# Kernel tuning notes

Measured on AMD Instinct MI355X. Metric: run time of the kernel, lower is better.

## Reference

```python
import jax, jax.numpy as jnp
import numpy as np

D_MODEL = 768
D_STATE = 16
D_CONV = 4
EXPAND = 2
D_INNER = D_MODEL * EXPAND
B, L = 2, 2048


def _silu(x):
    return x * jax.nn.sigmoid(x)


def _ssm_core(xn, inw, cw, cb, xw, dtw, dtb, Alog, Dp, outw):
    """Mamba selective SSM. xn: [B,L,d_model] -> [B,L,d_model]."""
    Bn, Ln, _ = xn.shape
    S = Alog.shape[1]
    d_inner = Alog.shape[0]
    k = cw.shape[-1]
    xz = xn @ inw                      # [B,L,2*d_inner]
    xi, z = jnp.split(xz, 2, axis=-1)
    # depthwise causal conv along L (torch pads both sides then slices [:L] == left-pad k-1)
    xc = jnp.swapaxes(xi, 1, 2)        # [B,d_inner,L]
    xc = jax.lax.conv_general_dilated(xc, cw, (1,), [(k - 1, 0)],
                                      feature_group_count=d_inner)
    xc = xc + cb[None, :, None]
    xc = _silu(jnp.swapaxes(xc, 1, 2))  # [B,L,d_inner]
    bcdt = xc @ xw                     # [B,L,1+2S]
    dt_raw = bcdt[..., :1]
    Bs = bcdt[..., 1:1 + S]            # [B,L,S]
    Cs = bcdt[..., 1 + S:]             # [B,L,S]
    dt = jax.nn.softplus(dt_raw * dtw[None, None, :] + dtb)  # [B,L,d_inner]
    A = -jnp.exp(jnp.clip(Alog, -6.0, 6.0))                  # [d_inner,S]
    dA = jnp.exp(dt[..., None] * A[None, None])               # [B,L,d_inner,S]
    dBx = dt[..., None] * Bs[:, :, None, :] * xc[..., None]   # [B,L,d_inner,S]

    def step(h, ins):
        dA_t, dBx_t, C_t = ins
        h = jnp.clip(dA_t * h + dBx_t, -10000.0, 10000.0)
        return h, jnp.einsum('bds,bs->bd', h, C_t)

    h0 = jnp.zeros((Bn, d_inner, S), xc.dtype)
    _, ys = jax.lax.scan(step, h0, (jnp.moveaxis(dA, 1, 0),
                                    jnp.moveaxis(dBx, 1, 0),
                                    jnp.moveaxis(Cs, 1, 0)))
    y = jnp.moveaxis(ys, 0, 1) + xc * Dp[None, None]
    y = y * _silu(z)
    return y @ outw


def setup_inputs() -> dict:
    key = jax.random.key(0)
    ks = jax.random.split(key, 20)
    def core_params(koff):
        return dict(
            inw=jax.random.normal(ks[koff + 0], (D_MODEL, 2 * D_INNER), jnp.float32) * 0.02,
            cw=jax.random.normal(ks[koff + 1], (D_INNER, 1, D_CONV), jnp.float32) * 0.2,
            cb=jnp.zeros((D_INNER,), jnp.float32),
            xw=jax.random.normal(ks[koff + 2], (D_INNER, 1 + 2 * D_STATE), jnp.float32) * 0.02,
            dtw=jax.random.normal(ks[koff + 3], (D_INNER,), jnp.float32) * 0.5,
            dtb=jax.random.normal(ks[koff + 4], (D_INNER,), jnp.float32) * 0.1,
            Alog=jnp.clip(jnp.log(jnp.arange(1, D_STATE + 1, dtype=jnp.float32))[None, :]
                          * jnp.ones((D_INNER, 1), jnp.float32), -6.0, 6.0),
            D=jnp.ones((D_INNER,), jnp.float32),
            outw=jax.random.normal(ks[koff + 5], (D_INNER, D_MODEL), jnp.float32) * 0.02,
        )
    f = core_params(2)
    b = core_params(8)
    return {
        'x': jax.random.normal(ks[0], (B, L, D_MODEL), jnp.float32),
        'ln_g': jnp.ones((D_MODEL,), jnp.float32),
        'ln_b': jnp.zeros((D_MODEL,), jnp.float32),
        'alpha': jnp.zeros((), jnp.float32),
        'f_inw': f['inw'], 'f_cw': f['cw'], 'f_cb': f['cb'], 'f_xw': f['xw'],
        'f_dtw': f['dtw'], 'f_dtb': f['dtb'], 'f_Alog': f['Alog'], 'f_D': f['D'], 'f_outw': f['outw'],
        'b_inw': b['inw'], 'b_cw': b['cw'], 'b_cb': b['cb'], 'b_xw': b['xw'],
        'b_dtw': b['dtw'], 'b_dtb': b['dtb'], 'b_Alog': b['Alog'], 'b_D': b['D'], 'b_outw': b['outw'],
    }


def reference(x, ln_g, ln_b, alpha,
              f_inw, f_cw, f_cb, f_xw, f_dtw, f_dtb, f_Alog, f_D, f_outw,
              b_inw, b_cw, b_cb, b_xw, b_dtw, b_dtb, b_Alog, b_D, b_outw):
    residual = x.astype(jnp.float32)
    mu = residual.mean(-1, keepdims=True)
    var = ((residual - mu) ** 2).mean(-1, keepdims=True)
    xn = (residual - mu) / jnp.sqrt(var + 1e-5) * ln_g + ln_b
    y_fwd = _ssm_core(xn, f_inw, f_cw, f_cb, f_xw, f_dtw, f_dtb, f_Alog, f_D, f_outw)
    y_bwd = jnp.flip(_ssm_core(jnp.flip(xn, 1), b_inw, b_cw, b_cb, b_xw,
                               b_dtw, b_dtb, b_Alog, b_D, b_outw), 1)
    a = jax.nn.sigmoid(alpha)
    y = a * y_fwd + (1.0 - a) * y_bwd
    return y + residual
```

## Files before the change

### kernel.cpp

```cpp
#include <hip/hip_runtime.h>
#include <cstddef>
#include <cstdint>

#define DMODEL 768
#define DINNER 1536
#define NSTATE 16
#define LSEQ   2048
#define NB     2
#define NTOK   (NB*LSEQ)
#define NBCDT  33

#define TC     32
#define NCHUNK (LSEQ/TC)
#define KSPLIT 12
#define LOG2E  1.44269504f

typedef __bf16 bf16x8 __attribute__((ext_vector_type(8)));
typedef float  floatx4 __attribute__((ext_vector_type(4)));

__device__ __forceinline__ float exp2_hw(float x) { return __builtin_amdgcn_exp2f(x); }
__device__ __forceinline__ float silu_f(float x) { return x / (1.f + expf(-x)); }
__device__ __forceinline__ float clip1e4(float x) {
    return __builtin_amdgcn_fmed3f(x, -1e4f, 1e4f);
}
__device__ __forceinline__ unsigned short f2bf(float f) {
    unsigned int u = __float_as_uint(f);
    unsigned int r = u + 0x7fffu + ((u >> 16) & 1u);
    return (unsigned short)(r >> 16);
}
__device__ __forceinline__ float bf2f(unsigned short u) {
    return __uint_as_float((unsigned int)u << 16);
}
__device__ __forceinline__ unsigned int pack2bf(float a, float b) {
    unsigned int ua = __float_as_uint(a); ua = ua + 0x7fffu + ((ua >> 16) & 1u);
    unsigned int ub = __float_as_uint(b); ub = ub + 0x7fffu + ((ub >> 16) & 1u);
    return (ua >> 16) | (ub & 0xffff0000u);
}
__device__ __forceinline__ void ld_lds16(unsigned short* lds, const unsigned short* g) {
    __builtin_amdgcn_global_load_lds(
        (const __attribute__((address_space(1))) unsigned int*)g,
        (__attribute__((address_space(3))) unsigned int*)lds,
        16, 0, 0);
}

__global__ void ln_kernel(const float* __restrict__ x,
                          const float* __restrict__ g,
                          const float* __restrict__ be,
                          unsigned short* __restrict__ xnb,
                          float* __restrict__ bcdt) {
    int row = blockIdx.x;
    int tid = threadIdx.x;
    int zi = row * 256 + tid;
    if (zi < 2 * NTOK * NBCDT) bcdt[zi] = 0.f;
    const float* xr = x + (size_t)row * DMODEL;
    float s = 0.f, ss = 0.f;
    for (int i = tid; i < DMODEL; i += 256) {
        float v = xr[i];
        s += v; ss += v * v;
    }
    for (int o = 32; o >= 1; o >>= 1) {
        s  += __shfl_xor(s,  o, 64);
        ss += __shfl_xor(ss, o, 64);
    }
    __shared__ float sS[4], sSS[4];
    int w = tid >> 6;
    if ((tid & 63) == 0) { sS[w] = s; sSS[w] = ss; }
    __syncthreads();
    s  = sS[0] + sS[1] + sS[2] + sS[3];
    ss = sSS[0] + sSS[1] + sSS[2] + sSS[3];
    float mu = s / DMODEL;
    float var = ss / DMODEL - mu * mu;
    float rstd = rsqrtf(var + 1e-5f);
    unsigned short* xo = xnb + (size_t)row * DMODEL;
    for (int i = tid; i < DMODEL; i += 256)
        xo[i] = f2bf((xr[i] - mu) * rstd * g[i] + be[i]);
}

__global__ __launch_bounds__(256)
void cast_weights(const float* __restrict__ f_inw, const float* __restrict__ b_inw,
                  const float* __restrict__ f_outw, const float* __restrict__ b_outw,
                  const float* __restrict__ f_xw, const float* __restrict__ b_xw,
                  const float* __restrict__ alpha,
                  unsigned short* __restrict__ inwT, unsigned short* __restrict__ outwT,
                  unsigned short* __restrict__ xwT) {
    __shared__ float t[32][33];
    int bid = blockIdx.x;
    int tid = threadIdx.x;
    int lr = tid >> 5, lc = tid & 31;
    if (bid < 4608) {
        int n0 = (bid % 192) * 32;
        int k0 = (bid / 192) * 32;
        const float* w = (n0 >= 3072) ? b_inw : f_inw;
        int nb = (n0 >= 3072) ? (n0 - 3072) : n0;
        #pragma unroll
        for (int r = 0; r < 4; r++)
            t[r * 8 + lr][lc] = w[(size_t)(k0 + r * 8 + lr) * 3072 + nb + lc];
        __syncthreads();
        #pragma unroll
        for (int r = 0; r < 4; r++)
            inwT[(size_t)(n0 + r * 8 + lr) * DMODEL + k0 + lc] = f2bf(t[lc][r * 8 + lr]);
    } else if (bid < 6912) {
        bid -= 4608;
        float a = 1.f / (1.f + expf(-alpha[0]));
        int n0 = (bid % 24) * 32;
        int k0 = (bid / 24) * 32;
        const float* w = (k0 >= DINNER) ? b_outw : f_outw;
        float sc = (k0 >= DINNER) ? (1.f - a) : a;
        int kb = (k0 >= DINNER) ? (k0 - DINNER) : k0;
        #pragma unroll
        for (int r = 0; r < 4; r++)
            t[r * 8 + lr][lc] = w[(size_t)(kb + r * 8 + lr) * DMODEL + n0 + lc];
        __syncthreads();
        #pragma unroll
        for (int r = 0; r < 4; r++)
            outwT[(size_t)(n0 + r * 8 + lr) * 3072 + k0 + lc] = f2bf(sc * t[lc][r * 8 + lr]);
    } else {
        bid -= 6912;
        int dir = bid / 48;
        int k0 = (bid % 48) * 32;
        const float* xw = dir ? b_xw : f_xw;
        unsigned short* dst = xwT + (size_t)dir * 48 * DINNER;
        for (int idx = tid; idx < 48 * 32; idx += 256) {
            int n = idx >> 5, kk = idx & 31;
            float v = (n < 33) ? xw[(size_t)(k0 + kk) * 33 + n] : 0.f;
            dst[(size_t)n * DINNER + k0 + kk] = f2bf(v);
        }
    }
}

__global__ __launch_bounds__(256)
void gemm_xz_mfma(const unsigned short* __restrict__ xnb,
                  const unsigned short* __restrict__ inwT,
                  unsigned short* __restrict__ xi, unsigned short* __restrict__ sz) {
    __shared__ unsigned short SH[2][2 * 128 * 64];
    int tid = threadIdx.x;
    int bm = blockIdx.y * 128;
    int bn = blockIdx.x * 128;
    int wave = tid >> 6, lane = tid & 63;
    int wm = (wave & 1) * 64, wn = (wave >> 1) * 64;
    int col15 = lane & 15, quad = lane >> 4;
    int lrow = lane >> 3;
    int lk   = (((lane & 7) ^ lrow) * 8);
    floatx4 acc[4][4];
    #pragma unroll
    for (int i = 0; i < 4; i++)
        #pragma unroll
        for (int j = 0; j < 4; j++)
            acc[i][j] = (floatx4){0.f, 0.f, 0.f, 0.f};

    int sw = col15 & 7;

#define STAGE_XZ(buf, k0)                                                       \
    {                                                                           \
        unsigned short* Abuf = SH[buf];                                         \
        unsigned short* Bbuf = SH[buf] + 128 * 64;                              \
        _Pragma("unroll")                                                       \
        for (int i = 0; i < 4; i++) {                                           \
            int r8 = wave * 32 + i * 8;                                         \
            int ra = r8 + lrow;                                                 \
            ld_lds16(&Abuf[r8 * 64], &xnb[(size_t)(bm + ra) * DMODEL + (k0) + lk]); \
            ld_lds16(&Bbuf[r8 * 64], &inwT[(size_t)(bn + ra) * DMODEL + (k0) + lk]); \
        }                                                                       \
    }

    STAGE_XZ(0, 0);
    __syncthreads();
    int cur = 0;
    for (int kt = 0; kt < DMODEL / 64; ++kt) {
        if (kt + 1 < DMODEL / 64) STAGE_XZ(cur ^ 1, (kt + 1) * 64);
        const unsigned short* Acur = SH[cur];
        const unsigned short* Bcur = SH[cur] + 128 * 64;
        #pragma unroll
        for (int k2 = 0; k2 < 2; k2++) {
            bf16x8 af[4], bf_[4];
            int pc = ((k2 * 4 + quad) ^ sw) * 8;
            #pragma unroll
            for (int mt = 0; mt < 4; mt++)
                af[mt] = *(const bf16x8*)(&Acur[(wm + mt * 16 + col15) * 64 + pc]);
            #pragma unroll
            for (int nt = 0; nt < 4; nt++)
                bf_[nt] = *(const bf16x8*)(&Bcur[(wn + nt * 16 + col15) * 64 + pc]);
            #pragma unroll
            for (int mt = 0; mt < 4; mt++)
                #pragma unroll
                for (int nt = 0; nt < 4; nt++)
                    acc[mt][nt] = __builtin_amdgcn_mfma_f32_16x16x32_bf16(
                        af[mt], bf_[nt], acc[mt][nt], 0, 0, 0);
        }
        __syncthreads();
        cur ^= 1;
    }
    int dirq = (bn >= 3072) ? 1 : 0;
    int cb0  = bn - dirq * 3072;
    int zs   = (cb0 >= DINNER) ? 1 : 0;
    int ccb  = cb0 - zs * DINNER;
    unsigned short* dst = zs ? sz : xi;
    unsigned short* C16 = &SH[0][0];
    #pragma unroll
    for (int mt = 0; mt < 4; mt++)
        #pragma unroll
        for (int nt = 0; nt < 4; nt++)
            #pragma unroll
            for (int r = 0; r < 4; r++) {
                int row = wm + mt * 16 + quad * 4 + r;
                int col = wn + nt * 16 + col15;
                float v = acc[mt][nt][r];
                if (zs) v = silu_f(v);
                C16[row * 136 + col] = f2bf(v);
            }
    __syncthreads();
    {
        int erow = tid >> 4;
        int cch  = tid & 15;
        size_t rowbase = (size_t)dirq * NTOK + bm;
        #pragma unroll
        for (int p = 0; p < 8; p++) {
            int row = p * 16 + erow;
            uint4 v = *(const uint4*)(&C16[row * 136 + cch * 8]);
            *(uint4*)(&dst[(rowbase + row) * DINNER + ccb + cch * 8]) = v;
        }
    }
#undef STAGE_XZ
}

__global__ __launch_bounds__(256)
void bcdt_conv_gemm_mfma(const unsigned short* __restrict__ xi,
                         const float* __restrict__ f_cw, const float* __restrict__ f_cb,
                         const float* __restrict__ b_cw, const float* __restrict__ b_cb,
                         const unsigned short* __restrict__ xwT,
                         float* __restrict__ bcdt,
                         unsigned short* __restrict__ xc) {
    __shared__ unsigned short Xs[131 * 64];
    __shared__ unsigned short As[128 * 64];
    __shared__ unsigned short Bs[48 * 64];
    int tid = threadIdx.x;
    int wave = tid >> 6, lane = tid & 63;
    int r0 = blockIdx.x * 128;
    int kc = blockIdx.y;
    int dirb = r0 >> 11;
    int dir = dirb >> 1, b = dirb & 1;
    int u0 = r0 & 2047;
    const float* cw = dir ? b_cw : f_cw;
    const float* cb = dir ? b_cb : f_cb;
    size_t xibase = ((size_t)dir * NTOK + (size_t)b * LSEQ) * DINNER;
    const unsigned short* Bsrc = xwT + (size_t)dir * 48 * DINNER;
    unsigned short* xcb = xc + (size_t)dirb * LSEQ * DINNER;

    int col15 = lane & 15, quad = lane >> 4;
    int sw = col15 & 7;
    int lrow = lane >> 3;
    int lcc = (lane & 7) * 8;
    int lk  = (((lane & 7) ^ lrow) * 8);
    int wm = wave * 32;

    int cp = (tid & 31) * 2;
    int rg = (tid >> 5) * 16;

    floatx4 acc[2][3];
    #pragma unroll
    for (int i = 0; i < 2; i++)
        #pragma unroll
        for (int j = 0; j < 3; j++)
            acc[i][j] = (floatx4){0.f, 0.f, 0.f, 0.f};

    for (int ks = 0; ks < 2; ks++) {
        int kb = kc * 128 + ks * 64;
        #pragma unroll
        for (int i = 0; i < 2; i++) {
            int g = wave + i * 4;
            if (g < 6)
                ld_lds16(&Bs[g * 8 * 64],
                         &Bsrc[(size_t)(g * 8 + lrow) * DINNER + kb + lk]);
        }
        #pragma unroll
        for (int i = 0; i < 4; i++) {
            int g = wave * 4 + i;
            int u = u0 + g * 8 + lrow;
            int l = dir ? (LSEQ - 1 - u) : u;
            ld_lds16(&Xs[(3 + g * 8) * 64], &xi[xibase + (size_t)l * DINNER + kb + lcc]);
        }
        if (tid < 96) {
            int hh = tid >> 5, c2 = (tid & 31) * 2;
            int u = u0 - 3 + hh;
            unsigned int v = 0;
            if (u >= 0) {
                int l = dir ? (LSEQ - 1 - u) : u;
                v = *(const unsigned int*)(&xi[xibase + (size_t)l * DINNER + kb + c2]);
            }
            *(unsigned int*)(&Xs[hh * 64 + c2]) = v;
        }
        __syncthreads();
        {
            int ch0 = kb + cp;
            float4 w0 = *(const float4*)(cw + (size_t)ch0 * 4);
            float4 w1 = *(const float4*)(cw + (size_t)(ch0 + 1) * 4);
            float cb0 = cb[ch0], cb1 = cb[ch0 + 1];
            unsigned int v;
            v = *(const unsigned int*)(&Xs[(rg + 0) * 64 + cp]);
            float a3 = bf2f((unsigned short)v), b3 = bf2f((unsigned short)(v >> 16));
            v = *(const unsigned int*)(&Xs[(rg + 1) * 64 + cp]);
            float a2 = bf2f((unsigned short)v), b2 = bf2f((unsigned short)(v >> 16));
            v = *(const unsigned int*)(&Xs[(rg + 2) * 64 + cp]);
            float a1 = bf2f((unsigned short)v), b1 = bf2f((unsigned short)(v >> 16));
            int cs = cp >> 3, e = cp & 7;
            #pragma unroll
            for (int j = 0; j < 16; j++) {
                int r = rg + j;
                v = *(const unsigned int*)(&Xs[(r + 3) * 64 + cp]);
                float a0 = bf2f((unsigned short)v), b0 = bf2f((unsigned short)(v >> 16));
                float xa = cb0;
                xa = fmaf(w0.x, a3, xa); xa = fmaf(w0.y, a2, xa);
                xa = fmaf(w0.z, a1, xa); xa = fmaf(w0.w, a0, xa);
                xa = silu_f(xa);
                float xb = cb1;
                xb = fmaf(w1.x, b3, xb); xb = fmaf(w1.y, b2, xb);
                xb = fmaf(w1.z, b1, xb); xb = fmaf(w1.w, b0, xb);
                xb = silu_f(xb);
                a3 = a2; a2 = a1; a1 = a0;
                b3 = b2; b2 = b1; b1 = b0;
                unsigned int pk = pack2bf(xa, xb);
                int ad = r * 64 + ((cs ^ (r & 7)) << 3) + e;
                *(unsigned int*)(&As[ad]) = pk;
                *(unsigned int*)(&xcb[(size_t)(u0 + r) * DINNER + ch0]) = pk;
            }
        }
        __syncthreads();
        #pragma unroll
        for (int k2 = 0; k2 < 2; k2++) {
            int pc = ((k2 * 4 + quad) ^ sw) * 8;
            bf16x8 af[2], bfr[3];
            #pragma unroll
            for (int mt = 0; mt < 2; mt++)
                af[mt] = *(const bf16x8*)(&As[(wm + mt * 16 + col15) * 64 + pc]);
            #pragma unroll
            for (int nt = 0; nt < 3; nt++)
                bfr[nt] = *(const bf16x8*)(&Bs[(nt * 16 + col15) * 64 + pc]);
            #pragma unroll
            for (int mt = 0; mt < 2; mt++)
                #pragma unroll
                for (int nt = 0; nt < 3; nt++)
                    acc[mt][nt] = __builtin_amdgcn_mfma_f32_16x16x32_bf16(
                        af[mt], bfr[nt], acc[mt][nt], 0, 0, 0);
        }
        __syncthreads();
    }
    #pragma unroll
    for (int mt = 0; mt < 2; mt++) {
        #pragma unroll
        for (int nt = 0; nt < 3; nt++) {
            int n = nt * 16 + col15;
            if (n < 33) {
                #pragma unroll
                for (int r = 0; r < 4; r++) {
                    int row = r0 + wm + mt * 16 + quad * 4 + r;
                    atomicAdd(&bcdt[(size_t)row * 33 + n], acc[mt][nt][r]);
                }
            }
        }
    }
}

__global__ __launch_bounds__(256, 4)
void scan_p1(const unsigned short* __restrict__ xc, const float* __restrict__ bcdt,
             const float* __restrict__ f_dtw, const float* __restrict__ f_dtb,
             const float* __restrict__ f_Alog,
             const float* __restrict__ b_dtw, const float* __restrict__ b_dtb,
             const float* __restrict__ b_Alog,
             float* __restrict__ Sdtbuf, float* __restrict__ hloc) {
    int tid = threadIdx.x;
    int d = blockIdx.x * 256 + tid;
    int chunk = blockIdx.y;
    int dirb  = blockIdx.z;
    int dir = dirb >> 1;
    const float* dtw  = dir ? b_dtw  : f_dtw;
    const float* dtb  = dir ? b_dtb  : f_dtb;
    const float* Alog = dir ? b_Alog : f_Alog;
    float dtw_d = dtw[d], dtb_d = dtb[d];
    float A2[NSTATE], h[NSTATE];
    #pragma unroll
    for (int s = 0; s < NSTATE; s++) {
        float al = fminf(fmaxf(Alog[d * NSTATE + s], -6.f), 6.f);
        A2[s] = -__expf(al) * LOG2E;
        h[s] = 0.f;
    }
    float Sdt = 0.f;
    int t0 = chunk * TC;
    const unsigned short* xp = xc + ((size_t)dirb * LSEQ + t0) * DINNER + d;
    size_t rbase = (size_t)dirb * LSEQ + (size_t)t0;
    const float* bc = bcdt + rbase * NBCDT;
    for (int t = 0; t < TC; t++) {
        float xv = bf2f(*xp); xp += DINNER;
        float dt_raw = bc[t * NBCDT];
        float u = fmaf(dt_raw, dtw_d, dtb_d);
        float dt = fmaxf(u, 0.f) + __logf(1.f + __expf(-fabsf(u)));
        Sdt += dt;
        float dtx = dt * xv;
        #pragma unroll
        for (int s = 0; s < NSTATE; s++) {
            float Bv = bc[t * NBCDT + 1 + s];
            h[s] = fmaf(exp2_hw(dt * A2[s]), h[s], dtx * Bv);
        }
    }
    Sdtbuf[(size_t)chunk * (4 * DINNER) + (size_t)dirb * DINNER + d] = Sdt;
    size_t base = ((size_t)chunk * 4 + dirb) * ((size_t)DINNER * NSTATE) + (size_t)d * NSTATE;
    #pragma unroll
    for (int s = 0; s < NSTATE; s++)
        hloc[base + s] = h[s];
}

__global__ void scan_p2(const float* __restrict__ Sdtbuf, float* __restrict__ hloc,
                        const float* __restrict__ f_Alog, const float* __restrict__ b_Alog) {
    int i = blockIdx.x * 256 + threadIdx.x;
    const int DS = DINNER * NSTATE;
    int dirb = i / DS;
    int rem = i - dirb * DS;
    int d = rem >> 4, s = rem & 15;
    const float* Alog = (dirb >> 1) ? b_Alog : f_Alog;
    float al = fminf(fmaxf(Alog[d * NSTATE + s], -6.f), 6.f);
    float A2 = -__expf(al) * LOG2E;
    float h = 0.f;
    const int stride = 4 * DS;
    const int sstr = 4 * DINNER;
    for (int c = 0; c < NCHUNK; c++) {
        size_t idx = (size_t)c * stride + i;
        float tmp = hloc[idx];
        hloc[idx] = h;
        float P = exp2_hw(A2 * Sdtbuf[(size_t)c * sstr + dirb * DINNER + d]);
        h = clip1e4(fmaf(P, h, tmp));
    }
}

__global__ __launch_bounds__(256, 4)
void scan_p3(const unsigned short* __restrict__ xc, const float* __restrict__ bcdt,
             const unsigned short* __restrict__ sz, const float* __restrict__ hpre,
             const float* __restrict__ f_dtw, const float* __restrict__ f_dtb,
             const float* __restrict__ f_Alog, const float* __restrict__ f_D,
             const float* __restrict__ b_dtw, const float* __restrict__ b_dtb,
             const float* __restrict__ b_Alog, const float* __restrict__ b_D,
             unsigned short* __restrict__ yvb) {
    int tid = threadIdx.x;
    int d = blockIdx.x * 256 + tid;
    int chunk = blockIdx.y;
    int dirb  = blockIdx.z;
    int dir = dirb >> 1, b = dirb & 1;
    const float* dtw  = dir ? b_dtw  : f_dtw;
    const float* dtb  = dir ? b_dtb  : f_dtb;
    const float* Alog = dir ? b_Alog : f_Alog;
    const float* Dp   = dir ? b_D    : f_D;
    float dtw_d = dtw[d], dtb_d = dtb[d], D_d = Dp[d];
    float A2[NSTATE], h[NSTATE];
    size_t hbase = ((size_t)chunk * 4 + dirb) * ((size_t)DINNER * NSTATE) + (size_t)d * NSTATE;
    #pragma unroll
    for (int s = 0; s < NSTATE; s++) {
        float al = fminf(fmaxf(Alog[d * NSTATE + s], -6.f), 6.f);
        A2[s] = -__expf(al) * LOG2E;
        h[s] = hpre[hbase + s];
    }
    int t0 = chunk * TC;
    const unsigned short* xp = xc + ((size_t)dirb * LSEQ + t0) * DINNER + d;
    size_t xbase = ((size_t)dir * NTOK + (size_t)b * LSEQ) * DINNER + d;
    long stride = dir ? -(long)DINNER : (long)DINNER;
    int l0 = dir ? (LSEQ - 1 - t0) : t0;
    const unsigned short* szp = sz + xbase + (size_t)l0 * DINNER;
    unsigned short* yp = yvb + ((size_t)(b * LSEQ + l0)) * 3072 + dir * DINNER + d;
    long ystride = stride * 2;
    size_t rbase = (size_t)dirb * LSEQ + (size_t)t0;
    const float* bc = bcdt + rbase * NBCDT;
    for (int t = 0; t < TC; t++) {
        float xv = bf2f(*xp); xp += DINNER;
        float dt_raw = bc[t * NBCDT];
        float u = fmaf(dt_raw, dtw_d, dtb_d);
        float dt = fmaxf(u, 0.f) + __logf(1.f + __expf(-fabsf(u)));
        float dtx = dt * xv;
        float p = 0.f;
        #pragma unroll
        for (int s = 0; s < NSTATE; s++) {
            float Bv = bc[t * NBCDT + 1 + s];
            float Cv = bc[t * NBCDT + 1 + NSTATE + s];
            h[s] = fmaf(exp2_hw(dt * A2[s]), h[s], dtx * Bv);
            p = fmaf(h[s], Cv, p);
        }
        float szv = bf2f(*szp); szp += stride;
        float y = (p + xv * D_d) * szv;
        *yp = f2bf(y); yp += ystride;
    }
}

__global__ __launch_bounds__(256)
void gemm_out_mfma(const unsigned short* __restrict__ yvb,
                   const unsigned short* __restrict__ outwT,
                   const float* __restrict__ x,
                   float* __restrict__ out) {
    __shared__ unsigned short SH[2][2 * 64 * 64];
    int tid = threadIdx.x;
    int bm = blockIdx.y * 64;
    int bn = blockIdx.x * 64;
    int wave = tid >> 6, lane = tid & 63;
    int wm = (wave & 1) * 32, wn = (wave >> 1) * 32;
    int col15 = lane & 15, quad = lane >> 4;
    int lrow = lane >> 3;
    int lk   = (((lane & 7) ^ lrow) * 8);
    floatx4 acc[2][2];
    #pragma unroll
    for (int i = 0; i < 2; i++)
        #pragma unroll
        for (int j = 0; j < 2; j++)
            acc[i][j] = (floatx4){0.f, 0.f, 0.f, 0.f};

    int sw = col15 & 7;

#define STAGE_OUT(buf, k0)                                                      \
    {                                                                           \
        unsigned short* Abuf = SH[buf];                                         \
        unsigned short* Bbuf = SH[buf] + 64 * 64;                               \
        _Pragma("unroll")                                                       \
        for (int i = 0; i < 2; i++) {                                           \
            int r8 = wave * 16 + i * 8;                                         \
            ld_lds16(&Abuf[r8 * 64], &yvb[(size_t)(bm + r8 + lrow) * 3072 + (k0) + lk]); \
            ld_lds16(&Bbuf[r8 * 64], &outwT[(size_t)(bn + r8 + lrow) * 3072 + (k0) + lk]); \
        }                                                                       \
    }

    STAGE_OUT(0, 0);
    __syncthreads();
    int cur = 0;
    for (int kt = 0; kt < 3072 / 64; ++kt) {
        if (kt + 1 < 3072 / 64) STAGE_OUT(cur ^ 1, (kt + 1) * 64);
        const unsigned short* Acur = SH[cur];
        const unsigned short* Bcur = SH[cur] + 64 * 64;
        #pragma unroll
        for (int k2 = 0; k2 < 2; k2++) {
            bf16x8 af[2], bf_[2];
            int pc = ((k2 * 4 + quad) ^ sw) * 8;
            #pragma unroll
            for (int mt = 0; mt < 2; mt++)
                af[mt] = *(const bf16x8*)(&Acur[(wm + mt * 16 + col15) * 64 + pc]);
            #pragma unroll
            for (int nt = 0; nt < 2; nt++)
                bf_[nt] = *(const bf16x8*)(&Bcur[(wn + nt * 16 + col15) * 64 + pc]);
            #pragma unroll
            for (int mt = 0; mt < 2; mt++)
                #pragma unroll
                for (int nt = 0; nt < 2; nt++)
                    acc[mt][nt] = __builtin_amdgcn_mfma_f32_16x16x32_bf16(
                        af[mt], bf_[nt], acc[mt][nt], 0, 0, 0);
        }
        __syncthreads();
        cur ^= 1;
    }
    #pragma unroll
    for (int mt = 0; mt < 2; mt++) {
        #pragma unroll
        for (int nt = 0; nt < 2; nt++) {
            #pragma unroll
            for (int r = 0; r < 4; r++) {
                int row = bm + wm + mt * 16 + quad * 4 + r;
                int gn  = bn + wn + nt * 16 + col15;
                out[(size_t)row * DMODEL + gn] = acc[mt][nt][r] + x[(size_t)row * DMODEL + gn];
            }
        }
    }
#undef STAGE_OUT
}

extern "C" void kernel_launch(void* const* d_in, const int* in_sizes, int n_in,
                              void* d_out, int out_size, void* d_ws, size_t ws_size,
                              hipStream_t stream) {
    const float* x     = (const float*)d_in[0];
    const float* ln_g  = (const float*)d_in[1];
    const float* ln_b  = (const float*)d_in[2];
    const float* alpha = (const float*)d_in[3];
    const float* f_inw  = (const float*)d_in[4];
    const float* f_cw   = (const float*)d_in[5];
    const float* f_cb   = (const float*)d_in[6];
    const float* f_xw   = (const float*)d_in[7];
    const float* f_dtw  = (const float*)d_in[8];
    const float* f_dtb  = (const float*)d_in[9];
    const float* f_Alog = (const float*)d_in[10];
    const float* f_D    = (const float*)d_in[11];
    const float* f_outw = (const float*)d_in[12];
    const float* b_inw  = (const float*)d_in[13];
    const float* b_cw   = (const float*)d_in[14];
    const float* b_cb   = (const float*)d_in[15];
    const float* b_xw   = (const float*)d_in[16];
    const float* b_dtw  = (const float*)d_in[17];
    const float* b_dtb  = (const float*)d_in[18];
    const float* b_Alog = (const float*)d_in[19];
    const float* b_D    = (const float*)d_in[20];
    const float* b_outw = (const float*)d_in[21];
    float* out = (float*)d_out;

    float* ws = (float*)d_ws;
    float* r_xnb  = ws;
    float* r_inwT = r_xnb + 1572864;
    float* r_outwT= r_inwT + 2359296;
    float* r_xib  = r_outwT + 1179648;
    float* r_szb  = r_xib + 6291456;
    float* r_yvb  = r_szb + 6291456;
    float* hloc   = r_yvb + 6291456;
    float* r_xc   = hloc + 6291456;
    float* Sdtbuf = r_xc + 6291456;
    float* bcdt   = Sdtbuf + 393216;

    unsigned short* xnb   = (unsigned short*)r_xnb;
    unsigned short* inwT  = (unsigned short*)r_inwT;
    unsigned short* outwT = (unsigned short*)r_outwT;
    unsigned short* xib   = (unsigned short*)r_xib;
    unsigned short* szb   = (unsigned short*)r_szb;
    unsigned short* yvb   = (unsigned short*)r_yvb;
    unsigned short* xcb   = (unsigned short*)r_xc;
    unsigned short* xwT   = (unsigned short*)hloc;

    ln_kernel<<<NTOK, 256, 0, stream>>>(x, ln_g, ln_b, xnb, bcdt);
    cast_weights<<<4608 + 2304 + 96, 256, 0, stream>>>(f_inw, b_inw, f_outw, b_outw,
                                                       f_xw, b_xw, alpha,
                                                       inwT, outwT, xwT);
    {
        dim3 grid(6144 / 128, NTOK / 128);
        gemm_xz_mfma<<<grid, 256, 0, stream>>>(xnb, inwT, xib, szb);
    }
    {
        dim3 g(2 * NTOK / 128, KSPLIT);
        bcdt_conv_gemm_mfma<<<g, 256, 0, stream>>>(xib, f_cw, f_cb, b_cw, b_cb,
                                                   xwT, bcdt, xcb);
    }
    {
        dim3 grid1(DINNER / 256, NCHUNK, 4);
        scan_p1<<<grid1, 256, 0, stream>>>(xcb, bcdt,
                                           f_dtw, f_dtb, f_Alog,
                                           b_dtw, b_dtb, b_Alog, Sdtbuf, hloc);
        scan_p2<<<(4 * DINNER * NSTATE) / 256, 256, 0, stream>>>(Sdtbuf, hloc,
                                                                 f_Alog, b_Alog);
        scan_p3<<<grid1, 256, 0, stream>>>(xcb, bcdt, szb, hloc,
                                           f_dtw, f_dtb, f_Alog, f_D,
                                           b_dtw, b_dtb, b_Alog, b_D, yvb);
    }
    {
        dim3 grid(DMODEL / 64, NTOK / 64);
        gemm_out_mfma<<<grid, 256, 0, stream>>>(yvb, outwT, x, out);
    }
}
```

Measured before the change: 361.3 us.

## Prefetch two K-tiles ahead in GEMMs with explicit vmcnt waits; double scan chunk

The in-projection and out-projection GEMM main loops now issue global-to-LDS loads two tiles ahead, using explicit s_waitcnt vmcnt counts and raw s_barrier in place of __syncthreads. This lets the next tile's loads stay in flight across compute instead of draining every iteration. The scan chunk length TC also doubles from 32 to 64, which halves the number of chunks in the chunked scan. The hand-counted vmcnt values must match the exact number of outstanding loads, or LDS data could be read before it arrives.

```diff
diff --git a/kernel.cpp b/kernel.cpp
--- a/kernel.cpp
+++ b/kernel.cpp
@@ -10,7 +10,7 @@
 #define NTOK   (NB*LSEQ)
 #define NBCDT  33
 
-#define TC     32
+#define TC     64
 #define NCHUNK (LSEQ/TC)
 #define KSPLIT 12
 #define LOG2E  1.44269504f
@@ -164,12 +164,13 @@
     }
 
     STAGE_XZ(0, 0);
-    __syncthreads();
-    int cur = 0;
+    STAGE_XZ(1, 64);
+    asm volatile("s_waitcnt vmcnt(8)" ::: "memory");
+    __builtin_amdgcn_sched_barrier(0);
+    __builtin_amdgcn_s_barrier();
     for (int kt = 0; kt < DMODEL / 64; ++kt) {
-        if (kt + 1 < DMODEL / 64) STAGE_XZ(cur ^ 1, (kt + 1) * 64);
-        const unsigned short* Acur = SH[cur];
-        const unsigned short* Bcur = SH[cur] + 128 * 64;
+        const unsigned short* Acur = SH[kt & 1];
+        const unsigned short* Bcur = SH[kt & 1] + 128 * 64;
         #pragma unroll
         for (int k2 = 0; k2 < 2; k2++) {
             bf16x8 af[4], bf_[4];
@@ -187,8 +188,15 @@
                     acc[mt][nt] = __builtin_amdgcn_mfma_f32_16x16x32_bf16(
                         af[mt], bf_[nt], acc[mt][nt], 0, 0, 0);
         }
-        __syncthreads();
-        cur ^= 1;
+        __builtin_amdgcn_s_barrier();
+        if (kt + 2 < DMODEL / 64) {
+            STAGE_XZ(kt & 1, (kt + 2) * 64);
+            asm volatile("s_waitcnt vmcnt(8)" ::: "memory");
+        } else {
+            asm volatile("s_waitcnt vmcnt(0)" ::: "memory");
+        }
+        __builtin_amdgcn_sched_barrier(0);
+        __builtin_amdgcn_s_barrier();
     }
     int dirq = (bn >= 3072) ? 1 : 0;
     int cb0  = bn - dirq * 3072;
@@ -522,12 +530,13 @@
     }
 
     STAGE_OUT(0, 0);
-    __syncthreads();
-    int cur = 0;
+    STAGE_OUT(1, 64);
+    asm volatile("s_waitcnt vmcnt(4)" ::: "memory");
+    __builtin_amdgcn_sched_barrier(0);
+    __builtin_amdgcn_s_barrier();
     for (int kt = 0; kt < 3072 / 64; ++kt) {
-        if (kt + 1 < 3072 / 64) STAGE_OUT(cur ^ 1, (kt + 1) * 64);
-        const unsigned short* Acur = SH[cur];
-        const unsigned short* Bcur = SH[cur] + 64 * 64;
+        const unsigned short* Acur = SH[kt & 1];
+        const unsigned short* Bcur = SH[kt & 1] + 64 * 64;
         #pragma unroll
         for (int k2 = 0; k2 < 2; k2++) {
             bf16x8 af[2], bf_[2];
@@ -545,8 +554,15 @@
                     acc[mt][nt] = __builtin_amdgcn_mfma_f32_16x16x32_bf16(
                         af[mt], bf_[nt], acc[mt][nt], 0, 0, 0);
         }
-        __syncthreads();
-        cur ^= 1;
+        __builtin_amdgcn_s_barrier();
+        if (kt + 2 < 3072 / 64) {
+            STAGE_OUT(kt & 1, (kt + 2) * 64);
+            asm volatile("s_waitcnt vmcnt(4)" ::: "memory");
+        } else {
+            asm volatile("s_waitcnt vmcnt(0)" ::: "memory");
+        }
+        __builtin_amdgcn_sched_barrier(0);
+        __builtin_amdgcn_s_barrier();
     }
     #pragma unroll
     for (int mt = 0; mt < 2; mt++) {
```

Measured after the change: 368.3 us. Within noise of the previous version (+1.9%).
